# Performance work log

Hardware: AMD Instinct MI355X
Metric: run time of the kernel (lower is better)

Reference implementation:

```python
import jax, jax.numpy as jnp
import numpy as np

NEG_SLOPE = 0.2


def gat_conv(x, src, dst, W, a_src, a_dst, b, concat):
    # x: [N, Fin]; W: [H*C, Fin]; a_src/a_dst: [H, C]; b: [H*C] or [C]
    N = x.shape[0]
    H, C = a_src.shape
    h = (x @ W.T).reshape(N, H, C)                      # per-head transform
    s_n = jnp.sum(h * a_src, axis=-1)                   # [N, H]
    d_n = jnp.sum(h * a_dst, axis=-1)                   # [N, H]
    e = jax.nn.leaky_relu(s_n[src] + d_n[dst], NEG_SLOPE)  # [E, H]
    # segment softmax over incoming edges of each destination node
    m = jax.ops.segment_max(e, dst, num_segments=N)
    m = jnp.where(jnp.isfinite(m), m, 0.0)
    ex = jnp.exp(e - m[dst])
    denom = jax.ops.segment_sum(ex, dst, num_segments=N)
    alpha = ex / (denom[dst] + 1e-16)                    # [E, H]
    msg = h[src] * alpha[:, :, None]                     # [E, H, C]
    out = jax.ops.segment_sum(msg, dst, num_segments=N)  # [N, H, C]
    out = out.reshape(N, H * C) if concat else out.mean(axis=1)
    return out + b


def setup_inputs() -> dict:
    key = jax.random.key(0)
    ks = jax.random.split(key, 16)
    N, E, F, C, H = 50000, 800000, 256, 128, 4
    sc = lambda fan_in: 1.0 / np.sqrt(fan_in)
    inp = {
        "x": jax.random.normal(ks[0], (N, F), dtype=jnp.float32),
        "edge_index": jax.random.randint(ks[1], (2, E), 0, N, dtype=jnp.int64),
        # layer 1: F -> H*C (concat)
        "W1": jax.random.normal(ks[2], (H * C, F), jnp.float32) * sc(F),
        "a_src1": jax.random.normal(ks[3], (H, C), jnp.float32) * sc(C),
        "a_dst1": jax.random.normal(ks[4], (H, C), jnp.float32) * sc(C),
        "b1": jnp.zeros((H * C,), jnp.float32),
        # layer 2: H*C -> H*C (concat)
        "W2": jax.random.normal(ks[5], (H * C, H * C), jnp.float32) * sc(H * C),
        "a_src2": jax.random.normal(ks[6], (H, C), jnp.float32) * sc(C),
        "a_dst2": jax.random.normal(ks[7], (H, C), jnp.float32) * sc(C),
        "b2": jnp.zeros((H * C,), jnp.float32),
        # layer 3: H*C -> C (heads=1, concat=False)
        "W3": jax.random.normal(ks[8], (C, H * C), jnp.float32) * sc(H * C),
        "a_src3": jax.random.normal(ks[9], (1, C), jnp.float32) * sc(C),
        "a_dst3": jax.random.normal(ks[10], (1, C), jnp.float32) * sc(C),
        "b3": jnp.zeros((C,), jnp.float32),
        # allocation head: C -> C//2 -> 1
        "Wh1": jax.random.normal(ks[11], (C // 2, C), jnp.float32) * sc(C),
        "bh1": jnp.zeros((C // 2,), jnp.float32),
        "Wh2": jax.random.normal(ks[12], (1, C // 2), jnp.float32) * sc(C // 2),
        "bh2": jnp.zeros((1,), jnp.float32),
    }
    return inp


def reference(x, edge_index, W1, a_src1, a_dst1, b1, W2, a_src2, a_dst2, b2,
              W3, a_src3, a_dst3, b3, Wh1, bh1, Wh2, bh2):
    N = x.shape[0]
    loops = jnp.arange(N, dtype=edge_index.dtype)
    src = jnp.concatenate([edge_index[0], loops])  # self-loops (PyG default)
    dst = jnp.concatenate([edge_index[1], loops])

    h = gat_conv(x, src, dst, W1, a_src1, a_dst1, b1, concat=True)
    h = jax.nn.elu(h)  # dropout is identity at inference
    h = gat_conv(h, src, dst, W2, a_src2, a_dst2, b2, concat=True)
    h = jax.nn.elu(h)
    embeddings = gat_conv(h, src, dst, W3, a_src3, a_dst3, b3, concat=False)

    z = jax.nn.relu(embeddings @ Wh1.T + bh1)
    allocation_scores = jax.nn.sigmoid(z @ Wh2.T + bh2)
    return embeddings, allocation_scores
```

## Files before the change

### kernel.cpp

```cpp
#include <hip/hip_runtime.h>
#include <math.h>

typedef _Float16 f16;
typedef f16 f16x2 __attribute__((ext_vector_type(2)));
typedef f16 f16x8 __attribute__((ext_vector_type(8)));
typedef float f32x4 __attribute__((ext_vector_type(4)));

template <int V> struct VecT;
template <> struct VecT<2> { using T = f16 __attribute__((ext_vector_type(2))); };
template <> struct VecT<8> { using T = f16 __attribute__((ext_vector_type(8))); };

__device__ __forceinline__ unsigned ordf(float f) {
  unsigned u = __float_as_uint(f);
  return (u >> 31) ? ~u : (u | 0x80000000u);
}
__device__ __forceinline__ float unordf(unsigned u) {
  return (u >> 31) ? __uint_as_float(u & 0x7fffffffu) : __uint_as_float(~u);
}


__global__ void k_count(const int* __restrict__ dstArr, int* __restrict__ cnt,
                        int E, int Et) {
  int i = blockIdx.x * blockDim.x + threadIdx.x;
  if (i >= Et) return;
  int d = (i < E) ? dstArr[i] : (i - E);
  atomicAdd(&cnt[d], 1);
}

__global__ __launch_bounds__(256) void k_scanA(const int* __restrict__ cnt,
                                               int* __restrict__ row_ptr,
                                               int* __restrict__ bsum, int n) {
  __shared__ int part[256];
  int t = threadIdx.x;
  int base = blockIdx.x * 1024 + t * 4;
  int4 v = make_int4(0, 0, 0, 0);
  if (base + 3 < n) v = *(const int4*)&cnt[base];
  else {
    if (base + 0 < n) v.x = cnt[base + 0];
    if (base + 1 < n) v.y = cnt[base + 1];
    if (base + 2 < n) v.z = cnt[base + 2];
    if (base + 3 < n) v.w = cnt[base + 3];
  }
  int s = v.x + v.y + v.z + v.w;
  part[t] = s;
  __syncthreads();
  for (int off = 1; off < 256; off <<= 1) {
    int x = (t >= off) ? part[t - off] : 0;
    __syncthreads();
    part[t] += x;
    __syncthreads();
  }
  int p0 = (t == 0) ? 0 : part[t - 1];
  int p1 = p0 + v.x, p2 = p1 + v.y, p3 = p2 + v.z;
  if (base + 0 < n) row_ptr[base + 0] = p0;
  if (base + 1 < n) row_ptr[base + 1] = p1;
  if (base + 2 < n) row_ptr[base + 2] = p2;
  if (base + 3 < n) row_ptr[base + 3] = p3;
  if (t == 255) bsum[blockIdx.x] = part[255];
}

__global__ __launch_bounds__(1024) void k_scanB(int* __restrict__ bsum, int nb) {
  __shared__ int part[1024];
  int t = threadIdx.x;
  int v = (t < nb) ? bsum[t] : 0;
  part[t] = v;
  __syncthreads();
  for (int off = 1; off < 1024; off <<= 1) {
    int x = (t >= off) ? part[t - off] : 0;
    __syncthreads();
    part[t] += x;
    __syncthreads();
  }
  if (t < nb) bsum[t] = (t == 0) ? 0 : part[t - 1];
  if (t == 1023) bsum[nb] = part[1023];
}

__global__ void k_scanC(int* __restrict__ row_ptr, int* __restrict__ cursor,
                        const int* __restrict__ bsum, int n, int nb) {
  int i = blockIdx.x * blockDim.x + threadIdx.x;
  if (i < n) {
    int v = row_ptr[i] + bsum[i >> 10];
    row_ptr[i] = v;
    cursor[i] = v;
  }
  if (i == n) row_ptr[n] = bsum[nb];
}

__global__ void k_fill(const int* __restrict__ dstArr,
                       const int* __restrict__ srcArr, int* __restrict__ cursor,
                       int* __restrict__ esrc, int E, int Et) {
  int i = blockIdx.x * blockDim.x + threadIdx.x;
  if (i >= Et) return;
  int d, s;
  if (i < E) { d = dstArr[i]; s = srcArr[i]; }
  else       { d = i - E; s = d; }
  int pos = atomicAdd(&cursor[d], 1);
  esrc[pos] = s;
}

__global__ void k_f2h4(const float* s0, f16* d0, int n0,
                       const float* s1, f16* d1, int n1,
                       const float* s2, f16* d2, int n2,
                       const float* s3, f16* d3, int n3) {
  int i = blockIdx.x * blockDim.x + threadIdx.x;
  const float* s; f16* d;
  if (i < n0) { s = s0; d = d0; }
  else if ((i -= n0) < n1) { s = s1; d = d1; }
  else if ((i -= n1) < n2) { s = s2; d = d2; }
  else if ((i -= n2) < n3) { s = s3; d = d3; }
  else return;
  float4 v = ((const float4*)s)[i];
  union { f16 h[4]; double dd; } u;
  u.h[0] = (f16)v.x; u.h[1] = (f16)v.y; u.h[2] = (f16)v.z; u.h[3] = (f16)v.w;
  ((double*)d)[i] = u.dd;
}

__global__ __launch_bounds__(256) void k_hgemm_nt(
    const f16* __restrict__ A, const f16* __restrict__ B,
    f16* __restrict__ C, int M, int Nn, int K, int nbx,
    const float* __restrict__ a_src, const float* __restrict__ a_dst,
    float* __restrict__ sArr, float* __restrict__ dArr,
    unsigned* __restrict__ gmaxU, int H) {
  __shared__ f16 As[2 * 128 * 32];
  __shared__ f16 Bs[2 * 128 * 32];
  int tid = threadIdx.x;
  int wave = tid >> 6, lane = tid & 63;
  int quad = lane >> 4, l16 = lane & 15;

  int nwg = gridDim.x;
  int orig = blockIdx.x;
  int q = nwg >> 3, r = nwg & 7;
  int xcd = orig & 7, pos = orig >> 3;
  int swz = (xcd < r) ? (xcd * (q + 1) + pos)
                      : (r * (q + 1) + (xcd - r) * q + pos);
  int bx = swz % nbx;
  int by = swz / nbx;
  int m0 = by * 128, n0 = bx * 128;
  int wm = (wave & 1) * 64, wn = (wave >> 1) * 64;

  int lr = lane >> 2;
  int lc = lane & 3;
  int chunk = lc ^ ((lr >> 1) & 3);
  int rb0 = wave * 16;
  int rb1 = 64 + wave * 16;
  int ga0 = m0 + rb0 + lr; if (ga0 >= M) ga0 = M - 1;
  int ga1 = m0 + rb1 + lr; if (ga1 >= M) ga1 = M - 1;
  const f16* gA0 = A + (size_t)ga0 * K + chunk * 8;
  const f16* gA1 = A + (size_t)ga1 * K + chunk * 8;
  const f16* gB0 = B + (size_t)(n0 + rb0 + lr) * K + chunk * 8;
  const f16* gB1 = B + (size_t)(n0 + rb1 + lr) * K + chunk * 8;

  int rsw = (quad ^ ((l16 >> 1) & 3)) * 8;
  const f16* Ard[4];
  const f16* Brd[4];
#pragma unroll
  for (int i = 0; i < 4; ++i) {
    Ard[i] = &As[(wm + i * 16 + l16) * 32 + rsw];
    Brd[i] = &Bs[(wn + i * 16 + l16) * 32 + rsw];
  }

  f32x4 acc[4][4];
#pragma unroll
  for (int i = 0; i < 4; ++i)
#pragma unroll
    for (int j = 0; j < 4; ++j) acc[i][j] = (f32x4)(0.f);

#define GLDS(gp, lp)                                                     \
  __builtin_amdgcn_global_load_lds(                                      \
      (const __attribute__((address_space(1))) void*)(gp),               \
      (__attribute__((address_space(3))) void*)(lp), 16, 0, 0)
#define STAGE(buf, kk)                                                   \
  do {                                                                   \
    GLDS(gA0 + (kk), As + (buf) * 4096 + rb0 * 32);                      \
    GLDS(gA1 + (kk), As + (buf) * 4096 + rb1 * 32);                      \
    GLDS(gB0 + (kk), Bs + (buf) * 4096 + rb0 * 32);                      \
    GLDS(gB1 + (kk), Bs + (buf) * 4096 + rb1 * 32);                      \
  } while (0)

  int nt = K >> 5;
  STAGE(0, 0);
  for (int t = 0; t < nt; ++t) {
    int cur = t & 1;
    if (t + 1 < nt) {
      STAGE(cur ^ 1, (t + 1) << 5);
      asm volatile("s_waitcnt vmcnt(4)\n\ts_barrier" ::: "memory");
    } else {
      asm volatile("s_waitcnt vmcnt(0)\n\ts_barrier" ::: "memory");
    }
    f16x8 af[4], bf[4];
#pragma unroll
    for (int i = 0; i < 4; ++i) af[i] = *(const f16x8*)(Ard[i] + cur * 4096);
#pragma unroll
    for (int j = 0; j < 4; ++j) bf[j] = *(const f16x8*)(Brd[j] + cur * 4096);
#pragma unroll
    for (int i = 0; i < 4; ++i)
#pragma unroll
      for (int j = 0; j < 4; ++j)
        acc[i][j] = __builtin_amdgcn_mfma_f32_16x16x32_f16(af[i], bf[j], acc[i][j], 0, 0, 0);
    asm volatile("s_barrier" ::: "memory");
  }
#undef STAGE
#undef GLDS

#pragma unroll
  for (int i = 0; i < 4; ++i) {
#pragma unroll
    for (int r = 0; r < 4; ++r) {
      int m = m0 + wm + i * 16 + quad * 4 + r;
      if (m < M) {
        f16* Cp = C + (size_t)m * Nn + n0 + wn + l16;
#pragma unroll
        for (int j = 0; j < 4; ++j) Cp[j * 16] = (f16)acc[i][j][r];
      }
    }
  }

  float av[4], ad[4];
#pragma unroll
  for (int j = 0; j < 4; ++j) {
    int col = n0 + wn + l16 + j * 16;
    av[j] = a_src[col];
    ad[j] = a_dst[col];
  }
  float sp[16], dp[16];
#pragma unroll
  for (int i = 0; i < 4; ++i)
#pragma unroll
    for (int r = 0; r < 4; ++r) {
      float ss = 0.f, dd = 0.f;
#pragma unroll
      for (int j = 0; j < 4; ++j) {
        ss += acc[i][j][r] * av[j];
        dd += acc[i][j][r] * ad[j];
      }
#pragma unroll
      for (int msk = 1; msk < 16; msk <<= 1) {
        ss += __shfl_xor(ss, msk);
        dd += __shfl_xor(dd, msk);
      }
      sp[i * 4 + r] = ss;
      dp[i * 4 + r] = dd;
    }

  __syncthreads();
  float* fb = (float*)As;
  int wv = wn >> 6;
  if (l16 == 0) {
#pragma unroll
    for (int i = 0; i < 4; ++i)
#pragma unroll
      for (int r = 0; r < 4; ++r) {
        int row = wm + i * 16 + quad * 4 + r;
        fb[wv * 128 + row] = sp[i * 4 + r];
        fb[256 + wv * 128 + row] = dp[i * 4 + r];
      }
  }
  __syncthreads();
  float sval = -3.0e38f;
  if (tid < 128) {
    int m = m0 + tid;
    if (m < M) {
      float s = fb[tid] + fb[128 + tid];
      float d = fb[256 + tid] + fb[384 + tid];
      int head = n0 >> 7;
      sArr[(size_t)m * H + head] = s;
      dArr[(size_t)m * H + head] = d;
      sval = s;
    }
  }
  float mx = sval;
#pragma unroll
  for (int msk = 32; msk; msk >>= 1) mx = fmaxf(mx, __shfl_xor(mx, msk));
  __syncthreads();
  if (lane == 0) fb[512 + wave] = mx;
  __syncthreads();
  if (tid == 0) {
    float m01 = fmaxf(fb[512], fb[513]);
    atomicMax(&gmaxU[n0 >> 7], ordf(m01));
  }
}

template <int HH, int CT, bool DOELU, typename OutT>
__global__ __launch_bounds__(256) void k_aggregate(
    const f16* __restrict__ hin, const float* __restrict__ sArr,
    const float* __restrict__ dArr, const int* __restrict__ row_ptr,
    const int* __restrict__ esrc, const unsigned* __restrict__ gmaxU,
    const float* __restrict__ bias, OutT* __restrict__ outp, int N, int E) {
  constexpr int VEC = CT / 64;
  constexpr int CPER = CT / HH;
  using gvec = typename VecT<VEC>::T;

  __shared__ int2 pairs[4][HH * 66];

  int wave = threadIdx.x >> 6;
  int lane = threadIdx.x & 63;
  int n = blockIdx.x * 4 + wave;
  if (n >= N) return;
  int e0 = row_ptr[n];
  int deg = row_ptr[n + 1] - e0;

  const int myhead = (HH == 1) ? 0 : (lane * VEC) / CPER;
  const int laneByte = lane * VEC * 2;

  float dloc[HH], mn[HH];
#pragma unroll
  for (int h = 0; h < HH; ++h) {
    dloc[h] = dArr[n * HH + h];
    float m = unordf(gmaxU[h]) + dloc[h];
    mn[h] = (m > 0.f) ? m : 0.2f * m;
  }

  float acc[VEC];
#pragma unroll
  for (int k = 0; k < VEC; ++k) acc[k] = 0.f;
  float dsum[HH];
#pragma unroll
  for (int h = 0; h < HH; ++h) dsum[h] = 0.f;

  int2* pw = &pairs[wave][0];
  const int2* pr = &pairs[wave][myhead * 66];

#define LOADG(VB, WB, g)                                                      \
  do {                                                                        \
    _Pragma("unroll") for (int j_ = 0; j_ < 4; ++j_) {                        \
      int2 p_ = pr[(g) * 4 + j_];                                             \
      WB[j_] = __int_as_float(p_.y);                                          \
      VB[j_] = *(const gvec*)((const char*)hin + (unsigned)(p_.x + laneByte));\
    }                                                                         \
  } while (0)

#define FMAG(VB, WB)                                                          \
  do {                                                                        \
    _Pragma("unroll") for (int j_ = 0; j_ < 4; ++j_)                          \
        _Pragma("unroll") for (int k_ = 0; k_ < VEC; ++k_)                    \
            acc[k_] += WB[j_] * (float)VB[j_][k_];                            \
  } while (0)

  for (int base = 0; base < deg; base += 64) {
    int cn = min(64, deg - base);

    int soff = 0;
    float w_l[HH];
#pragma unroll
    for (int h = 0; h < HH; ++h) w_l[h] = 0.f;
    if (lane < cn) {
      int s = esrc[e0 + base + lane];
      soff = s * (CT * 2);
      if (HH == 4) {
        float4 sv = ((const float4*)sArr)[s];
        float svv[4] = {sv.x, sv.y, sv.z, sv.w};
#pragma unroll
        for (int h = 0; h < 4; ++h) {
          float e = svv[h] + dloc[h];
          e = (e > 0.f) ? e : 0.2f * e;
          w_l[h] = __expf(e - mn[h]);
        }
      } else {
        float e = sArr[s] + dloc[0];
        e = (e > 0.f) ? e : 0.2f * e;
        w_l[0] = __expf(e - mn[0]);
      }
    }
#pragma unroll
    for (int h = 0; h < HH; ++h) dsum[h] += w_l[h];

#pragma unroll
    for (int h = 0; h < HH; ++h)
      pw[h * 66 + lane] = make_int2(soff, __float_as_int(w_l[h]));
    asm volatile("s_waitcnt lgkmcnt(0)" ::: "memory");

    int cng = (cn + 3) >> 2;
    gvec vA[4], vB[4];
    float wA[4], wB[4];
    LOADG(vA, wA, 0);
    int g = 0;
    while (g + 2 < cng) {
      LOADG(vB, wB, g + 1);
      FMAG(vA, wA);
      LOADG(vA, wA, g + 2);
      FMAG(vB, wB);
      g += 2;
    }
    if (g + 1 < cng) {
      LOADG(vB, wB, g + 1);
      FMAG(vA, wA);
      FMAG(vB, wB);
    } else {
      FMAG(vA, wA);
    }
  }
#undef LOADG
#undef FMAG

  float dn;
  if (HH == 4) {
    float t0 = dsum[0], t1 = dsum[1], t2 = dsum[2], t3 = dsum[3];
#pragma unroll
    for (int m = 1; m < 64; m <<= 1) {
      t0 += __shfl_xor(t0, m);
      t1 += __shfl_xor(t1, m);
      t2 += __shfl_xor(t2, m);
      t3 += __shfl_xor(t3, m);
    }
    dn = (myhead < 2) ? (myhead == 0 ? t0 : t1) : (myhead == 2 ? t2 : t3);
  } else {
    float t0 = dsum[0];
#pragma unroll
    for (int m = 1; m < 64; m <<= 1) t0 += __shfl_xor(t0, m);
    dn = t0;
  }
  dn += 1e-16f;

  struct alignas(sizeof(OutT) * VEC) OutV { OutT v[VEC]; } ov;
#pragma unroll
  for (int k = 0; k < VEC; ++k) {
    float v = acc[k] / dn + bias[lane * VEC + k];
    if (DOELU) v = (v > 0.f) ? v : expm1f(v);
    ov.v[k] = (OutT)v;
  }
  *(OutV*)(outp + (size_t)n * CT + lane * VEC) = ov;
}

__global__ __launch_bounds__(256) void k_head(
    const float* __restrict__ emb, const float* __restrict__ Wh1,
    const float* __restrict__ bh1, const float* __restrict__ Wh2,
    const float* __restrict__ bh2, float* __restrict__ scores, int N) {
  __shared__ float w1s[64 * 132];
  __shared__ float w2s[64];
  __shared__ float b1s[64];
  int t = threadIdx.x;
  for (int i = t; i < 64 * 32; i += 256) {
    int r = i >> 5, c4 = i & 31;
    float4 v = ((const float4*)Wh1)[i];
    *(float4*)&w1s[r * 132 + c4 * 4] = v;
  }
  if (t < 64) { w2s[t] = Wh2[t]; b1s[t] = bh1[t]; }
  __syncthreads();
  float b2v = bh2[0];
  int wave = t >> 6, lane = t & 63;
  int gw = blockIdx.x * 4 + wave;
  int nw = gridDim.x * 4;
  for (int n = gw; n < N; n += nw) {
    float2 xv = ((const float2*)(emb + (size_t)n * 128))[lane];
    float z = b1s[lane];
#pragma unroll
    for (int j = 0; j < 32; ++j) {
      float4 w = *(const float4*)&w1s[lane * 132 + 4 * j];
      float a0 = __shfl(xv.x, 2 * j);
      float a1 = __shfl(xv.y, 2 * j);
      float a2 = __shfl(xv.x, 2 * j + 1);
      float a3 = __shfl(xv.y, 2 * j + 1);
      z += w.x * a0 + w.y * a1 + w.z * a2 + w.w * a3;
    }
    z = fmaxf(z, 0.f);
    float v = z * w2s[lane];
#pragma unroll
    for (int off = 32; off; off >>= 1) v += __shfl_down(v, off);
    if (lane == 0) scores[n] = 1.f / (1.f + __expf(-(v + b2v)));
  }
}


extern "C" void kernel_launch(void* const* d_in, const int* in_sizes, int n_in,
                              void* d_out, int out_size, void* d_ws, size_t ws_size,
                              hipStream_t stream) {
  const float* x   = (const float*)d_in[0];
  const int*   ei  = (const int*)d_in[1];
  const float* W1  = (const float*)d_in[2];
  const float* as1 = (const float*)d_in[3];
  const float* ad1 = (const float*)d_in[4];
  const float* b1  = (const float*)d_in[5];
  const float* W2  = (const float*)d_in[6];
  const float* as2 = (const float*)d_in[7];
  const float* ad2 = (const float*)d_in[8];
  const float* b2  = (const float*)d_in[9];
  const float* W3  = (const float*)d_in[10];
  const float* as3 = (const float*)d_in[11];
  const float* ad3 = (const float*)d_in[12];
  const float* b3  = (const float*)d_in[13];
  const float* Wh1 = (const float*)d_in[14];
  const float* bh1 = (const float*)d_in[15];
  const float* Wh2 = (const float*)d_in[16];
  const float* bh2 = (const float*)d_in[17];
  float* out = (float*)d_out;

  const int F = 256, HC = 512, H = 4, C = 128;
  const int N = in_sizes[0] / F;
  const int E = in_sizes[1] / 2;
  const int Et = E + N;
  const int* srcArr = ei;
  const int* dstArr = ei + E;

  char* ws = (char*)d_ws;
  size_t off = 0;
  auto alloc = [&](size_t bytes) -> void* {
    void* p = ws + off;
    off += (bytes + 255) & ~(size_t)255;
    return p;
  };
  f16*   h16    = (f16*)alloc((size_t)N * HC * 2);
  f16*   hAgg   = (f16*)alloc((size_t)N * HC * 2);
  f16*   xh     = (f16*)alloc((size_t)N * F * 2);
  f16*   W1h    = (f16*)alloc((size_t)HC * F * 2);
  f16*   W2h    = (f16*)alloc((size_t)HC * HC * 2);
  f16*   W3h    = (f16*)alloc((size_t)C * HC * 2);
  int* row_ptr  = (int*)alloc((size_t)(N + 1) * 4);
  char* zr      = (char*)alloc((size_t)N * 4 + 64);
  int* cnt      = (int*)zr;
  unsigned* gm1 = (unsigned*)(zr + (size_t)N * 4);
  unsigned* gm2 = gm1 + 4;
  unsigned* gm3 = gm1 + 8;
  int* cursor   = (int*)alloc((size_t)N * 4);
  int* esrc     = (int*)alloc((size_t)Et * 4);
  float* sArr   = (float*)alloc((size_t)N * H * 4);
  float* dArr   = (float*)alloc((size_t)N * H * 4);
  int* bsum     = (int*)alloc((size_t)1028 * 4);
  (void)ws_size; (void)n_in; (void)out_size;

  hipMemsetAsync(zr, 0, (size_t)N * 4 + 64, stream);
  int eb = (Et + 255) / 256;
  int nb = (N + 1023) / 1024;
  k_count<<<eb, 256, 0, stream>>>(dstArr, cnt, E, Et);
  k_scanA<<<nb, 256, 0, stream>>>(cnt, row_ptr, bsum, N);
  k_scanB<<<1, 1024, 0, stream>>>(bsum, nb);
  k_scanC<<<(N + 256) / 256, 256, 0, stream>>>(row_ptr, cursor, bsum, N, nb);
  k_fill<<<eb, 256, 0, stream>>>(dstArr, srcArr, cursor, esrc, E, Et);

  int c0 = N * F / 4, c1 = HC * F / 4, c2 = HC * HC / 4, c3 = C * HC / 4;
  int ctot = c0 + c1 + c2 + c3;
  k_f2h4<<<(ctot + 255) / 256, 256, 0, stream>>>(x, xh, c0, W1, W1h, c1,
                                                 W2, W2h, c2, W3, W3h, c3);

  int aggGrid = (N + 3) / 4;
  int mblk = (N + 127) / 128;
  int nblk1 = 4 * mblk;
  int nblk3 = mblk;

  k_hgemm_nt<<<nblk1, 256, 0, stream>>>(xh, W1h, h16, N, HC, F, 4,
                                        as1, ad1, sArr, dArr, gm1, H);
  k_aggregate<4, 512, true, f16><<<aggGrid, 256, 0, stream>>>(
      h16, sArr, dArr, row_ptr, esrc, gm1, b1, hAgg, N, E);

  k_hgemm_nt<<<nblk1, 256, 0, stream>>>(hAgg, W2h, h16, N, HC, HC, 4,
                                        as2, ad2, sArr, dArr, gm2, H);
  k_aggregate<4, 512, true, f16><<<aggGrid, 256, 0, stream>>>(
      h16, sArr, dArr, row_ptr, esrc, gm2, b2, hAgg, N, E);

  k_hgemm_nt<<<nblk3, 256, 0, stream>>>(hAgg, W3h, h16, N, C, HC, 1,
                                        as3, ad3, sArr, dArr, gm3, 1);
  k_aggregate<1, 128, false, float><<<aggGrid, 256, 0, stream>>>(
      h16, sArr, dArr, row_ptr, esrc, gm3, b3, out, N, E);

  k_head<<<512, 256, 0, stream>>>(out, Wh1, bh1, Wh2, bh2, out + (size_t)N * C, N);
}
```

Measured before the change: 759.1 us.

## Triple-buffer GEMM LDS staging and split edges across half-waves in single-head aggregate

The fp16 GEMM goes from double to triple buffering of LDS tiles, issuing loads two k-steps ahead to hide global latency better, at the cost of more shared memory per block. The single-head aggregation kernel now gives each half-wave alternate edges with 4-wide vector loads, instead of the whole wave reading 2-wide vectors for one edge at a time. The two half-wave partial sums are combined with a shuffle before output. This doubles the number of edge gathers in flight and widens each load.

```diff
diff --git a/kernel.cpp b/kernel.cpp
--- a/kernel.cpp
+++ b/kernel.cpp
@@ -3,11 +3,13 @@
 
 typedef _Float16 f16;
 typedef f16 f16x2 __attribute__((ext_vector_type(2)));
+typedef f16 f16x4 __attribute__((ext_vector_type(4)));
 typedef f16 f16x8 __attribute__((ext_vector_type(8)));
 typedef float f32x4 __attribute__((ext_vector_type(4)));
 
 template <int V> struct VecT;
 template <> struct VecT<2> { using T = f16 __attribute__((ext_vector_type(2))); };
+template <> struct VecT<4> { using T = f16 __attribute__((ext_vector_type(4))); };
 template <> struct VecT<8> { using T = f16 __attribute__((ext_vector_type(8))); };
 
 __device__ __forceinline__ unsigned ordf(float f) {
@@ -121,8 +123,8 @@
     const float* __restrict__ a_src, const float* __restrict__ a_dst,
     float* __restrict__ sArr, float* __restrict__ dArr,
     unsigned* __restrict__ gmaxU, int H) {
-  __shared__ f16 As[2 * 128 * 32];
-  __shared__ f16 Bs[2 * 128 * 32];
+  __shared__ f16 As[3 * 4096];
+  __shared__ f16 Bs[3 * 4096];
   int tid = threadIdx.x;
   int wave = tid >> 6, lane = tid & 63;
   int quad = lane >> 4, l16 = lane & 15;
@@ -176,31 +178,40 @@
     GLDS(gB0 + (kk), Bs + (buf) * 4096 + rb0 * 32);                      \
     GLDS(gB1 + (kk), Bs + (buf) * 4096 + rb1 * 32);                      \
   } while (0)
+#define COMPUTE(bufidx)                                                       \
+  do {                                                                        \
+    f16x8 af[4], bf[4];                                                       \
+    _Pragma("unroll") for (int i_ = 0; i_ < 4; ++i_)                          \
+        af[i_] = *(const f16x8*)(Ard[i_] + (bufidx) * 4096);                  \
+    _Pragma("unroll") for (int j_ = 0; j_ < 4; ++j_)                          \
+        bf[j_] = *(const f16x8*)(Brd[j_] + (bufidx) * 4096);                  \
+    _Pragma("unroll") for (int i_ = 0; i_ < 4; ++i_)                          \
+        _Pragma("unroll") for (int j_ = 0; j_ < 4; ++j_)                      \
+            acc[i_][j_] = __builtin_amdgcn_mfma_f32_16x16x32_f16(             \
+                af[i_], bf[j_], acc[i_][j_], 0, 0, 0);                        \
+  } while (0)
 
   int nt = K >> 5;
   STAGE(0, 0);
-  for (int t = 0; t < nt; ++t) {
-    int cur = t & 1;
-    if (t + 1 < nt) {
-      STAGE(cur ^ 1, (t + 1) << 5);
-      asm volatile("s_waitcnt vmcnt(4)\n\ts_barrier" ::: "memory");
-    } else {
-      asm volatile("s_waitcnt vmcnt(0)\n\ts_barrier" ::: "memory");
-    }
-    f16x8 af[4], bf[4];
-#pragma unroll
-    for (int i = 0; i < 4; ++i) af[i] = *(const f16x8*)(Ard[i] + cur * 4096);
-#pragma unroll
-    for (int j = 0; j < 4; ++j) bf[j] = *(const f16x8*)(Brd[j] + cur * 4096);
-#pragma unroll
-    for (int i = 0; i < 4; ++i)
-#pragma unroll
-      for (int j = 0; j < 4; ++j)
-        acc[i][j] = __builtin_amdgcn_mfma_f32_16x16x32_f16(af[i], bf[j], acc[i][j], 0, 0, 0);
+  STAGE(1, 32);
+  int cur = 0, sb = 2;
+  for (int t = 0; t + 2 < nt; ++t) {
+    STAGE(sb, (t + 2) << 5);
+    asm volatile("s_waitcnt vmcnt(8)\n\ts_barrier" ::: "memory");
+    COMPUTE(cur);
     asm volatile("s_barrier" ::: "memory");
-  }
+    cur = (cur == 2) ? 0 : cur + 1;
+    sb = (sb == 2) ? 0 : sb + 1;
+  }
+  asm volatile("s_waitcnt vmcnt(4)\n\ts_barrier" ::: "memory");
+  COMPUTE(cur);
+  asm volatile("s_barrier" ::: "memory");
+  cur = (cur == 2) ? 0 : cur + 1;
+  asm volatile("s_waitcnt vmcnt(0)\n\ts_barrier" ::: "memory");
+  COMPUTE(cur);
 #undef STAGE
 #undef GLDS
+#undef COMPUTE
 
 #pragma unroll
   for (int i = 0; i < 4; ++i) {
@@ -286,7 +297,7 @@
     const float* __restrict__ dArr, const int* __restrict__ row_ptr,
     const int* __restrict__ esrc, const unsigned* __restrict__ gmaxU,
     const float* __restrict__ bias, OutT* __restrict__ outp, int N, int E) {
-  constexpr int VEC = CT / 64;
+  constexpr int VEC = (HH == 1) ? 4 : (CT / 64);
   constexpr int CPER = CT / HH;
   using gvec = typename VecT<VEC>::T;
 
@@ -300,7 +311,8 @@
   int deg = row_ptr[n + 1] - e0;
 
   const int myhead = (HH == 1) ? 0 : (lane * VEC) / CPER;
-  const int laneByte = lane * VEC * 2;
+  const int l32 = lane & 31, half = lane >> 5;
+  const int laneByte = (HH == 1) ? l32 * 8 : lane * VEC * 2;
 
   float dloc[HH], mn[HH];
 #pragma unroll
@@ -320,10 +332,11 @@
   int2* pw = &pairs[wave][0];
   const int2* pr = &pairs[wave][myhead * 66];
 
+#define PIDX(g, j) ((HH == 1) ? ((g) * 8 + (j) * 2 + half) : ((g) * 4 + (j)))
 #define LOADG(VB, WB, g)                                                      \
   do {                                                                        \
     _Pragma("unroll") for (int j_ = 0; j_ < 4; ++j_) {                        \
-      int2 p_ = pr[(g) * 4 + j_];                                             \
+      int2 p_ = pr[PIDX(g, j_)];                                              \
       WB[j_] = __int_as_float(p_.y);                                          \
       VB[j_] = *(const gvec*)((const char*)hin + (unsigned)(p_.x + laneByte));\
     }                                                                         \
@@ -369,7 +382,7 @@
       pw[h * 66 + lane] = make_int2(soff, __float_as_int(w_l[h]));
     asm volatile("s_waitcnt lgkmcnt(0)" ::: "memory");
 
-    int cng = (cn + 3) >> 2;
+    int cng = (HH == 1) ? ((cn + 7) >> 3) : ((cn + 3) >> 2);
     gvec vA[4], vB[4];
     float wA[4], wB[4];
     LOADG(vA, wA, 0);
@@ -391,6 +404,12 @@
   }
 #undef LOADG
 #undef FMAG
+#undef PIDX
+
+  if (HH == 1) {
+#pragma unroll
+    for (int k = 0; k < VEC; ++k) acc[k] += __shfl_xor(acc[k], 32);
+  }
 
   float dn;
   if (HH == 4) {
@@ -411,14 +430,27 @@
   }
   dn += 1e-16f;
 
-  struct alignas(sizeof(OutT) * VEC) OutV { OutT v[VEC]; } ov;
-#pragma unroll
-  for (int k = 0; k < VEC; ++k) {
-    float v = acc[k] / dn + bias[lane * VEC + k];
-    if (DOELU) v = (v > 0.f) ? v : expm1f(v);
-    ov.v[k] = (OutT)v;
-  }
-  *(OutV*)(outp + (size_t)n * CT + lane * VEC) = ov;
+  if (HH == 1) {
+    if (lane < 32) {
+      struct alignas(16) OutV { OutT v[4]; } ov;
+#pragma unroll
+      for (int k = 0; k < 4; ++k) {
+        float v = acc[k] / dn + bias[l32 * 4 + k];
+        if (DOELU) v = (v > 0.f) ? v : expm1f(v);
+        ov.v[k] = (OutT)v;
+      }
+      *(OutV*)(outp + (size_t)n * CT + l32 * 4) = ov;
+    }
+  } else {
+    struct alignas(sizeof(OutT) * VEC) OutV { OutT v[VEC]; } ov;
+#pragma unroll
+    for (int k = 0; k < VEC; ++k) {
+      float v = acc[k] / dn + bias[lane * VEC + k];
+      if (DOELU) v = (v > 0.f) ? v : expm1f(v);
+      ov.v[k] = (OutT)v;
+    }
+    *(OutV*)(outp + (size_t)n * CT + lane * VEC) = ov;
+  }
 }
 
 __global__ __launch_bounds__(256) void k_head(
```

Result: faster. 743.5 us (-2.1%).
